# Optimization experiments

Hardware: AMD Instinct MI355X
Metric: run time of the kernel (lower is better)

## Reference

```python
import jax, jax.numpy as jnp
import numpy as np

EPS = 1e-5


def setup_inputs() -> dict:
    key = jax.random.key(0)
    ks = jax.random.split(key, 6)
    B, C, H, W = 32, 256, 32, 32
    T, O, K, KS = 256, 256, 4, 3
    return {
        "x": jax.random.normal(ks[0], (B, C, H, W), dtype=jnp.float32),
        "z": jax.random.normal(ks[1], (B, T), dtype=jnp.float32),
        "w1": jax.random.normal(ks[2], (T, T + C), dtype=jnp.float32) * 0.05,
        "bn_gamma": jnp.ones((T,), jnp.float32),
        "bn_beta": jnp.zeros((T,), jnp.float32),
        "bn_mean": jnp.zeros((T,), jnp.float32),
        "bn_var": jnp.ones((T,), jnp.float32),
        "w2": jax.random.normal(ks[3], (K, T), dtype=jnp.float32) * 0.05,
        "weight": jax.random.normal(ks[4], (K, O, C, KS, KS), dtype=jnp.float32) * 0.05,
        "static_weight": jax.random.normal(ks[5], (O, C, KS, KS), dtype=jnp.float32) * 0.05,
    }


def _kernel_attention(x, z, w1, bn_gamma, bn_beta, bn_mean, bn_var, w2):
    # x: [B,C,H,W], z: [B,T] -> att: [B,K]
    avg = jnp.mean(x, axis=(2, 3))                 # adaptive avg pool to 1x1 -> [B,C]
    a = jnp.concatenate([z, avg], axis=1)          # [B, T+C]
    h = a @ w1.T                                   # 1x1 conv on 1x1 spatial == matmul
    h = (h - bn_mean) / jnp.sqrt(bn_var + EPS) * bn_gamma + bn_beta  # BN (eval)
    h = jax.nn.relu(h)
    att = h @ w2.T                                 # [B,K]
    return jax.nn.sigmoid(att)                     # temperature = 1.0


def reference(x, z, w1, bn_gamma, bn_beta, bn_mean, bn_var, w2, weight, static_weight):
    B = x.shape[0]
    att = _kernel_attention(x, z, w1, bn_gamma, bn_beta, bn_mean, bn_var, w2)  # [B,K]
    # per-sample mixed weights: [B,O,C,k,k]
    agg_w = jnp.einsum('bk,koihw->boihw', att, weight * 0.1) + static_weight[None]

    def conv_one(xi, wi):
        # xi: [C,H,W], wi: [O,C,k,k]
        out = jax.lax.conv_general_dilated(
            xi[None], wi, window_strides=(1, 1), padding=[(1, 1), (1, 1)],
            dimension_numbers=('NCHW', 'OIHW', 'NCHW'))
        return out[0]

    return jax.vmap(conv_one)(x, agg_w)            # [B,O,H,W]
```

## Files before the change

### kernel.cpp

```cpp
#include <hip/hip_runtime.h>
#include <hip/hip_bf16.h>

typedef __attribute__((ext_vector_type(4))) float f32x4;
typedef __attribute__((ext_vector_type(8))) short bf16x8;
typedef __attribute__((ext_vector_type(8))) unsigned short ushort8;

#define EPSBN 1e-5f

__device__ __forceinline__ unsigned short f2bf(float f) {
  unsigned int u = __builtin_bit_cast(unsigned int, f);
  u += 0x7fffu + ((u >> 16) & 1u);
  return (unsigned short)(u >> 16);
}

__device__ __forceinline__ void gload_lds16(const unsigned short* g, unsigned short* l) {
  __builtin_amdgcn_global_load_lds(
      (const __attribute__((address_space(1))) void*)g,
      (__attribute__((address_space(3))) void*)l, 16, 0, 0);
}

__global__ __launch_bounds__(256) void prep_kernel(const float* __restrict__ x,
                                                   float* __restrict__ avg,
                                                   unsigned short* __restrict__ xpad) {
  int blk = blockIdx.x;
  int b = blk >> 5, cg = blk & 31;
  int t = threadIdx.x;
  int c = t >> 5, l32 = t & 31;
  __shared__ unsigned short lds_t[1024 * 9];
  __shared__ float avg_lds[8];
  const float4* xb4 = reinterpret_cast<const float4*>(x) + ((size_t)(b * 256 + cg * 8 + c)) * 256;
  float s = 0.f;
#pragma unroll
  for (int i = 0; i < 8; ++i) {
    float4 v = xb4[l32 + 32 * i];
    s += v.x + v.y + v.z + v.w;
    int p = 4 * (l32 + 32 * i);
    lds_t[(p + 0) * 9 + c] = f2bf(v.x);
    lds_t[(p + 1) * 9 + c] = f2bf(v.y);
    lds_t[(p + 2) * 9 + c] = f2bf(v.z);
    lds_t[(p + 3) * 9 + c] = f2bf(v.w);
  }
#pragma unroll
  for (int off = 16; off >= 1; off >>= 1) s += __shfl_down(s, off, 32);
  if (l32 == 0) avg_lds[c] = s;
  __syncthreads();
  if (t < 8) avg[b * 256 + cg * 8 + t] = avg_lds[t] * (1.0f / 1024.0f);
  size_t obase = (size_t)blk * 1156 * 8;
  for (int sIdx = t; sIdx < 1156; sIdx += 256) {
    int h = sIdx / 34, w = sIdx % 34;
    ushort8 v;
    if (h >= 1 && h <= 32 && w >= 1 && w <= 32) {
      int p = (h - 1) * 32 + (w - 1);
#pragma unroll
      for (int cl = 0; cl < 8; ++cl) v[cl] = lds_t[p * 9 + cl];
    } else {
#pragma unroll
      for (int cl = 0; cl < 8; ++cl) v[cl] = 0;
    }
    *reinterpret_cast<ushort8*>(xpad + obase + (size_t)sIdx * 8) = v;
  }
}

__global__ __launch_bounds__(256) void att_kernel(
    const float* __restrict__ z, const float* __restrict__ avg,
    const float* __restrict__ w1, const float* __restrict__ gamma,
    const float* __restrict__ beta, const float* __restrict__ mean,
    const float* __restrict__ var, const float* __restrict__ w2,
    float* __restrict__ att) {
  int b = blockIdx.x, t = threadIdx.x;
  __shared__ __align__(16) float a[512];
  __shared__ float h[256];
  a[t] = z[b * 256 + t];
  a[t + 256] = avg[b * 256 + t];
  __syncthreads();
  const float4* wr = reinterpret_cast<const float4*>(w1 + (size_t)t * 512);
  const float4* a4 = reinterpret_cast<const float4*>(a);
  float s = 0.f;
#pragma unroll 4
  for (int j = 0; j < 128; ++j) {
    float4 wv = wr[j], av = a4[j];
    s += wv.x * av.x + wv.y * av.y + wv.z * av.z + wv.w * av.w;
  }
  s = (s - mean[t]) * rsqrtf(var[t] + EPSBN) * gamma[t] + beta[t];
  h[t] = fmaxf(s, 0.f);
  __syncthreads();
  int wv_ = t >> 6, lane = t & 63;
  const float* w2r = w2 + wv_ * 256;
  float p = h[lane] * w2r[lane] + h[lane + 64] * w2r[lane + 64] +
            h[lane + 128] * w2r[lane + 128] + h[lane + 192] * w2r[lane + 192];
#pragma unroll
  for (int off = 32; off >= 1; off >>= 1) p += __shfl_down(p, off);
  if (lane == 0) att[b * 4 + wv_] = 1.0f / (1.0f + expf(-p));
}

#define MROW 291
__global__ __launch_bounds__(256) void mix_kernel(
    const float* __restrict__ weight, const float* __restrict__ statw,
    const float* __restrict__ att, unsigned short* __restrict__ agg) {
  int cc = blockIdx.x >> 5;
  int og = blockIdx.x & 31;
  int o0 = og * 8;
  int t = threadIdx.x;
  __shared__ float ldsf[5][8][MROW];
  __shared__ float att_lds[128];
  if (t < 128) att_lds[t] = att[t];
  const float* bases[5] = {statw, weight, weight + 589824, weight + 2 * 589824,
                           weight + 3 * 589824};
#pragma unroll
  for (int i = 0; i < 12; ++i) {
    int L = i * 256 + t;
    if (L < 2880) {
      int a = L / 576;
      int r = L % 576;
      int o_l = r / 72;
      int q = r % 72;
      float4 v = *reinterpret_cast<const float4*>(bases[a] + (size_t)(o0 + o_l) * 2304 +
                                                  cc * 288 + q * 4);
      float* d = &ldsf[a][o_l][q * 4];
      d[0] = v.x; d[1] = v.y; d[2] = v.z; d[3] = v.w;
    }
  }
  __syncthreads();
  for (int slot = t; slot < 288; slot += 256) {
    int o_l = slot & 7;
    int cblk = (slot >> 3) & 3;
    int tap = slot >> 5;
    float sv[8], wk0[8], wk1[8], wk2[8], wk3[8];
#pragma unroll
    for (int cl = 0; cl < 8; ++cl) {
      int idx9 = (cblk * 8 + cl) * 9 + tap;
      sv[cl] = ldsf[0][o_l][idx9];
      wk0[cl] = ldsf[1][o_l][idx9];
      wk1[cl] = ldsf[2][o_l][idx9];
      wk2[cl] = ldsf[3][o_l][idx9];
      wk3[cl] = ldsf[4][o_l][idx9];
    }
    size_t obase = ((size_t)(tap * 8 + cc) * 4 + cblk) * 256 + (o0 + o_l);
    for (int b = 0; b < 32; ++b) {
      float a0 = 0.1f * att_lds[b * 4 + 0];
      float a1 = 0.1f * att_lds[b * 4 + 1];
      float a2 = 0.1f * att_lds[b * 4 + 2];
      float a3 = 0.1f * att_lds[b * 4 + 3];
      ushort8 outv;
#pragma unroll
      for (int cl = 0; cl < 8; ++cl) {
        float v = sv[cl] + a0 * wk0[cl] + a1 * wk1[cl] + a2 * wk2[cl] + a3 * wk3[cl];
        outv[cl] = f2bf(v);
      }
      *reinterpret_cast<ushort8*>(agg + ((size_t)b * 73728 + obase) * 8) = outv;
    }
  }
}

__global__ __launch_bounds__(256, 4) void conv_kernel(
    const unsigned short* __restrict__ xpad, const unsigned short* __restrict__ agg,
    float* __restrict__ out) {
  int wgid = (blockIdx.x & 7) * 128 + (blockIdx.x >> 3);
  int b = wgid >> 5;
  int r = wgid & 31;
  int ot = r >> 3;
  int pt = r & 7;
  int h0 = pt * 4;

  __shared__ __align__(16) unsigned short x_lds[2][4 * 2048];

  int tid = threadIdx.x;
  int lane = tid & 63, wv = tid >> 6;
  int wave_mo = (wv & 1) * 32;
  int wave_no = (wv >> 1) * 64;
  int kb = lane >> 4, ln = lane & 15;

  f32x4 acc[2][4];
#pragma unroll
  for (int i = 0; i < 2; ++i)
#pragma unroll
    for (int j = 0; j < 4; ++j) acc[i][j] = (f32x4){0.f, 0.f, 0.f, 0.f};

  const unsigned short* aggL =
      agg + (size_t)b * 589824 + ((size_t)kb * 256 + ot * 64 + wave_mo + ln) * 8;

  auto issueX = [&](int cc, int bsel) {
    const unsigned short* g = xpad + ((size_t)(b * 32 + cc * 4 + wv) * 1156 + h0 * 34) * 8;
    unsigned short* l = &x_lds[bsel][wv * 2048];
#pragma unroll
    for (int i = 0; i < 4; ++i) gload_lds16(g + i * 512 + lane * 8, l + i * 512);
  };
  auto loadA = [&](int tg, bf16x8* dst) {
    const unsigned short* g = aggL + (size_t)tg * 8192;
    dst[0] = *reinterpret_cast<const bf16x8*>(g);
    dst[1] = *reinterpret_cast<const bf16x8*>(g + 128);
  };

  issueX(0, 0);
  bf16x8 A0[2], A1[2], A2[2];
  loadA(0 * 8 + 0, A0);
  loadA(1 * 8 + 0, A1);
  __syncthreads();

#pragma unroll 1
  for (int cc = 0; cc < 8; ++cc) {
    const unsigned short* xb = &x_lds[cc & 1][kb * 2048];
#pragma unroll
    for (int tap = 0; tap < 9; ++tap) {
      if (tap < 7) {
        loadA((tap + 2) * 8 + cc, A2);
      } else if (cc < 7) {
        loadA((tap - 7) * 8 + (cc + 1), A2);
      }
      if (tap == 7 && cc < 7) issueX(cc + 1, (cc + 1) & 1);
      int dh = tap / 3, dw = tap % 3;
      bf16x8 bfr[4];
#pragma unroll
      for (int bj = 0; bj < 4; ++bj) {
        int p = wave_no + bj * 16 + ln;
        int rr = (p >> 5) + dh;
        int wc = (p & 31) + dw;
        bfr[bj] = *reinterpret_cast<const bf16x8*>(xb + (rr * 34 + wc) * 8);
      }
      __builtin_amdgcn_s_setprio(1);
#pragma unroll
      for (int ai = 0; ai < 2; ++ai)
#pragma unroll
        for (int bj = 0; bj < 4; ++bj)
          acc[ai][bj] =
              __builtin_amdgcn_mfma_f32_16x16x32_bf16(A0[ai], bfr[bj], acc[ai][bj], 0, 0, 0);
      __builtin_amdgcn_s_setprio(0);
#pragma unroll
      for (int ai = 0; ai < 2; ++ai) {
        A0[ai] = A1[ai];
        A1[ai] = A2[ai];
      }
    }
    __syncthreads();
  }

  size_t ob = ((size_t)b * 256 + ot * 64 + wave_mo) * 1024 + (size_t)pt * 128 + wave_no;
#pragma unroll
  for (int ai = 0; ai < 2; ++ai)
#pragma unroll
    for (int bj = 0; bj < 4; ++bj) {
#pragma unroll
      for (int v = 0; v < 4; ++v) {
        int oo = ai * 16 + (lane >> 4) * 4 + v;
        out[ob + (size_t)oo * 1024 + bj * 16 + ln] = acc[ai][bj][v];
      }
    }
}

extern "C" void kernel_launch(void* const* d_in, const int* in_sizes, int n_in,
                              void* d_out, int out_size, void* d_ws, size_t ws_size,
                              hipStream_t stream) {
  const float* x = (const float*)d_in[0];
  const float* z = (const float*)d_in[1];
  const float* w1 = (const float*)d_in[2];
  const float* gamma = (const float*)d_in[3];
  const float* beta = (const float*)d_in[4];
  const float* mean = (const float*)d_in[5];
  const float* var = (const float*)d_in[6];
  const float* w2 = (const float*)d_in[7];
  const float* weight = (const float*)d_in[8];
  const float* statw = (const float*)d_in[9];
  float* out = (float*)d_out;

  float* att = (float*)d_ws;
  float* avg = (float*)((char*)d_ws + 1024);
  unsigned short* xpad = (unsigned short*)((char*)d_ws + 65536);
  unsigned short* agg = (unsigned short*)((char*)d_ws + 19009536);

  prep_kernel<<<1024, 256, 0, stream>>>(x, avg, xpad);
  att_kernel<<<32, 256, 0, stream>>>(z, avg, w1, gamma, beta, mean, var, w2, att);
  mix_kernel<<<256, 256, 0, stream>>>(weight, statw, att, agg);
  conv_kernel<<<1024, 256, 0, stream>>>(xpad, agg, out);
}
```

Before: 86.68 us.

## Enlarge conv workgroup to cover all output channels and stage full input tile

The conv kernel now uses 512-thread workgroups that each compute all 256 output channels for one batch and a 4-row pixel strip, rather than splitting output channels across four workgroups. The whole 32-channel-group input strip (128 KB) is loaded into LDS once up front, which removes the double-buffered per-stage loads and per-stage barriers. This cuts redundant input loads across output tiles and doubles the per-wave accumulator tile to 64x64. In exchange LDS use and register pressure rise sharply, occupancy falls to a single 256-block grid, and the up-front load is no longer overlapped with compute.

```diff
diff --git a/kernel.cpp b/kernel.cpp
--- a/kernel.cpp
+++ b/kernel.cpp
@@ -152,54 +152,53 @@
   }
 }
 
-__global__ __launch_bounds__(256, 4) void conv_kernel(
+__global__ __launch_bounds__(512, 2) void conv_kernel(
     const unsigned short* __restrict__ xpad, const unsigned short* __restrict__ agg,
     float* __restrict__ out) {
-  int wgid = (blockIdx.x & 7) * 128 + (blockIdx.x >> 3);
-  int b = wgid >> 5;
-  int r = wgid & 31;
-  int ot = r >> 3;
-  int pt = r & 7;
+  int wgid = (blockIdx.x & 7) * 32 + (blockIdx.x >> 3);
+  int pt = wgid & 7;
+  int b = wgid >> 3;
   int h0 = pt * 4;
 
-  __shared__ __align__(16) unsigned short x_lds[2][4 * 2048];
+  __shared__ __align__(16) unsigned short x_lds[32 * 2048];
 
   int tid = threadIdx.x;
   int lane = tid & 63, wv = tid >> 6;
-  int wave_mo = (wv & 1) * 32;
-  int wave_no = (wv >> 1) * 64;
+  int wave_mo = (wv >> 1) * 64;
+  int wave_no = (wv & 1) * 64;
   int kb = lane >> 4, ln = lane & 15;
 
-  f32x4 acc[2][4];
-#pragma unroll
-  for (int i = 0; i < 2; ++i)
+  f32x4 acc[4][4];
+#pragma unroll
+  for (int i = 0; i < 4; ++i)
 #pragma unroll
     for (int j = 0; j < 4; ++j) acc[i][j] = (f32x4){0.f, 0.f, 0.f, 0.f};
 
   const unsigned short* aggL =
-      agg + (size_t)b * 589824 + ((size_t)kb * 256 + ot * 64 + wave_mo + ln) * 8;
-
-  auto issueX = [&](int cc, int bsel) {
-    const unsigned short* g = xpad + ((size_t)(b * 32 + cc * 4 + wv) * 1156 + h0 * 34) * 8;
-    unsigned short* l = &x_lds[bsel][wv * 2048];
-#pragma unroll
-    for (int i = 0; i < 4; ++i) gload_lds16(g + i * 512 + lane * 8, l + i * 512);
-  };
+      agg + (size_t)b * 589824 + ((size_t)kb * 256 + wave_mo + ln) * 8;
   auto loadA = [&](int tg, bf16x8* dst) {
     const unsigned short* g = aggL + (size_t)tg * 8192;
-    dst[0] = *reinterpret_cast<const bf16x8*>(g);
-    dst[1] = *reinterpret_cast<const bf16x8*>(g + 128);
+#pragma unroll
+    for (int i = 0; i < 4; ++i) dst[i] = *reinterpret_cast<const bf16x8*>(g + i * 128);
   };
 
-  issueX(0, 0);
-  bf16x8 A0[2], A1[2], A2[2];
-  loadA(0 * 8 + 0, A0);
-  loadA(1 * 8 + 0, A1);
+#pragma unroll
+  for (int si = 0; si < 4; ++si) {
+    int s = wv * 4 + si;
+    const unsigned short* g = xpad + ((size_t)(b * 32 + s) * 1156 + h0 * 34) * 8;
+    unsigned short* l = &x_lds[s * 2048];
+#pragma unroll
+    for (int i = 0; i < 4; ++i) gload_lds16(g + i * 512 + lane * 8, l + i * 512);
+  }
+
+  bf16x8 A0[4], A1[4], A2[4];
+  loadA(0, A0);
+  loadA(8, A1);
   __syncthreads();
 
 #pragma unroll 1
   for (int cc = 0; cc < 8; ++cc) {
-    const unsigned short* xb = &x_lds[cc & 1][kb * 2048];
+    const unsigned short* xb = &x_lds[(cc * 4 + kb) * 2048];
 #pragma unroll
     for (int tap = 0; tap < 9; ++tap) {
       if (tap < 7) {
@@ -207,7 +206,6 @@
       } else if (cc < 7) {
         loadA((tap - 7) * 8 + (cc + 1), A2);
       }
-      if (tap == 7 && cc < 7) issueX(cc + 1, (cc + 1) & 1);
       int dh = tap / 3, dw = tap % 3;
       bf16x8 bfr[4];
 #pragma unroll
@@ -217,26 +215,23 @@
         int wc = (p & 31) + dw;
         bfr[bj] = *reinterpret_cast<const bf16x8*>(xb + (rr * 34 + wc) * 8);
       }
-      __builtin_amdgcn_s_setprio(1);
-#pragma unroll
-      for (int ai = 0; ai < 2; ++ai)
+#pragma unroll
+      for (int ai = 0; ai < 4; ++ai)
 #pragma unroll
         for (int bj = 0; bj < 4; ++bj)
           acc[ai][bj] =
               __builtin_amdgcn_mfma_f32_16x16x32_bf16(A0[ai], bfr[bj], acc[ai][bj], 0, 0, 0);
-      __builtin_amdgcn_s_setprio(0);
-#pragma unroll
-      for (int ai = 0; ai < 2; ++ai) {
+#pragma unroll
+      for (int ai = 0; ai < 4; ++ai) {
         A0[ai] = A1[ai];
         A1[ai] = A2[ai];
       }
     }
-    __syncthreads();
-  }
-
-  size_t ob = ((size_t)b * 256 + ot * 64 + wave_mo) * 1024 + (size_t)pt * 128 + wave_no;
-#pragma unroll
-  for (int ai = 0; ai < 2; ++ai)
+  }
+
+  size_t ob = ((size_t)b * 256 + wave_mo) * 1024 + (size_t)pt * 128 + wave_no;
+#pragma unroll
+  for (int ai = 0; ai < 4; ++ai)
 #pragma unroll
     for (int bj = 0; bj < 4; ++bj) {
 #pragma unroll
@@ -270,5 +265,5 @@
   prep_kernel<<<1024, 256, 0, stream>>>(x, avg, xpad);
   att_kernel<<<32, 256, 0, stream>>>(z, avg, w1, gamma, beta, mean, var, w2, att);
   mix_kernel<<<256, 256, 0, stream>>>(weight, statw, att, agg);
-  conv_kernel<<<1024, 256, 0, stream>>>(xpad, agg, out);
-}
+  conv_kernel<<<256, 512, 0, stream>>>(xpad, agg, out);
+}
```

Result: slower. 93.16 us (+7.5%).
